# Optimization experiments

Measured on AMD Instinct MI355X. Metric: run time of the kernel, lower is better.

The kernel has to match this reference:

```python
import jax, jax.numpy as jnp
import numpy as np

N = 50000
E = 800000
F_IN = 256
HID = 96
N_CLS = 32
NEG_SLOPE = 0.2


def setup_inputs() -> dict:
    key = jax.random.key(0)
    ks = jax.random.split(key, 10)
    x = jax.random.normal(ks[0], (N, F_IN), dtype=jnp.float32)
    edge_index = jax.random.randint(ks[1], (2, E), 0, N, dtype=jnp.int64)
    s1 = 1.0 / np.sqrt(F_IN)
    s2 = 1.0 / np.sqrt(HID)
    return {
        "x": x,
        "edge_index": edge_index,
        "W1": jax.random.normal(ks[2], (F_IN, HID), dtype=jnp.float32) * s1,
        "a1_src": jax.random.normal(ks[3], (HID,), dtype=jnp.float32) * s2,
        "a1_dst": jax.random.normal(ks[4], (HID,), dtype=jnp.float32) * s2,
        "b1": jnp.zeros((HID,), dtype=jnp.float32),
        "W2": jax.random.normal(ks[5], (HID, N_CLS), dtype=jnp.float32) * s2,
        "a2_src": jax.random.normal(ks[6], (N_CLS,), dtype=jnp.float32) * (1.0 / np.sqrt(N_CLS)),
        "a2_dst": jax.random.normal(ks[7], (N_CLS,), dtype=jnp.float32) * (1.0 / np.sqrt(N_CLS)),
        "b2": jnp.zeros((N_CLS,), dtype=jnp.float32),
    }


def _gat_conv(x, src, dst, W, a_src, a_dst, b, n_nodes):
    # single-head GATConv (PyG defaults), self-loops already in src/dst
    h = x @ W                                  # [N, out]
    alpha_src = h @ a_src                      # [N]
    alpha_dst = h @ a_dst                      # [N]
    e = alpha_src[src] + alpha_dst[dst]        # [E'] edge logits (msg j->i: dst groups)
    e = jnp.where(e > 0, e, NEG_SLOPE * e)     # leaky_relu
    # segment softmax over edges grouped by destination node
    m = jax.ops.segment_max(e, dst, num_segments=n_nodes)
    ex = jnp.exp(e - m[dst])
    denom = jax.ops.segment_sum(ex, dst, num_segments=n_nodes)
    alpha = ex / denom[dst]                    # [E']
    out = jax.ops.segment_sum(alpha[:, None] * h[src], dst, num_segments=n_nodes)
    return out + b


def reference(x, edge_index, W1, a1_src, a1_dst, b1, W2, a2_src, a2_dst, b2):
    loops = jnp.arange(N, dtype=edge_index.dtype)
    src = jnp.concatenate([edge_index[0], loops])
    dst = jnp.concatenate([edge_index[1], loops])
    h = _gat_conv(x, src, dst, W1, a1_src, a1_dst, b1, N)
    h = jax.nn.elu(h)
    # dropout omitted (eval mode, training=False)
    out = _gat_conv(h, src, dst, W2, a2_src, a2_dst, b2, N)
    return jax.nn.log_softmax(out, axis=1)
```

## Files before the change

### kernel.cpp

```cpp
#include <hip/hip_runtime.h>
#include <cstdint>
#include <cstddef>

#define NNODES 50000
#define NEDGES 800000
#define MEDGES (NEDGES + NNODES)
#define FIN    256
#define HID    96
#define NCLS   32
#define NEG_SLOPE 0.2f

#define NBUCK  391
#define BCAP   3072

typedef unsigned int uint32;
typedef __attribute__((ext_vector_type(8))) short short8;
typedef __attribute__((ext_vector_type(4))) float f32x4;

__device__ __forceinline__ ushort bf_round(float f) {
    uint32 u = __float_as_uint(f);
    u += 0x7FFFu + ((u >> 16) & 1u);
    return (ushort)(u >> 16);
}
__device__ __forceinline__ uint32 pack_bf16x2(float a, float b) {
    return (uint32)bf_round(a) | ((uint32)bf_round(b) << 16);
}
__device__ __forceinline__ float bf_lo(uint32 u) { return __uint_as_float(u << 16); }
__device__ __forceinline__ float bf_hi(uint32 u) { return __uint_as_float(u & 0xFFFF0000u); }
__device__ __forceinline__ float lrelu(float t) { return (t > 0.f) ? t : NEG_SLOPE * t; }
__device__ __forceinline__ float af(int i) { return __int_as_float(i); }


__global__ __launch_bounds__(256) void bucket1_kernel(const int* __restrict__ ei,
                                                      int* __restrict__ gcount,
                                                      int2* __restrict__ staging) {
    __shared__ int hist[NBUCK];
    __shared__ int base_sh[NBUCK];
    for (int i = threadIdx.x; i < NBUCK; i += 256) hist[i] = 0;
    __syncthreads();

    int s[8], d[8], rk[8], bk[8];
    int e0 = blockIdx.x * 2048;
#pragma unroll
    for (int i = 0; i < 8; ++i) {
        int e = e0 + i * 256 + threadIdx.x;
        if (e < MEDGES) {
            if (e < NEDGES) { s[i] = ei[e]; d[i] = ei[NEDGES + e]; }
            else            { s[i] = e - NEDGES; d[i] = s[i]; }
            bk[i] = d[i] >> 7;
            rk[i] = atomicAdd(&hist[bk[i]], 1);
        } else bk[i] = -1;
    }
    __syncthreads();
    for (int i = threadIdx.x; i < NBUCK; i += 256) {
        int c = hist[i];
        base_sh[i] = c ? atomicAdd(&gcount[i], c) : 0;
    }
    __syncthreads();
#pragma unroll
    for (int i = 0; i < 8; ++i) {
        if (bk[i] >= 0) {
            int pos = base_sh[bk[i]] + rk[i];
            if (pos < BCAP)
                staging[(size_t)bk[i] * BCAP + pos] = make_int2(s[i], d[i]);
        }
    }
}

__global__ __launch_bounds__(512) void bscan_kernel(const int* __restrict__ gcount,
                                                    int* __restrict__ bbase) {
    __shared__ int sd[512];
    int t = threadIdx.x;
    int v = (t < NBUCK) ? gcount[t] : 0;
    sd[t] = v;
    __syncthreads();
    for (int off = 1; off < 512; off <<= 1) {
        int val = (t >= off) ? sd[t - off] : 0;
        __syncthreads();
        sd[t] += val;
        __syncthreads();
    }
    if (t < NBUCK) bbase[t] = sd[t] - v;
}

__global__ __launch_bounds__(256) void bucket2_kernel(const int2* __restrict__ staging,
                                                      const int* __restrict__ gcount,
                                                      const int* __restrict__ bbase,
                                                      int* __restrict__ rowptr,
                                                      int* __restrict__ esrc) {
    __shared__ int dcount[128];
    __shared__ int dincl[128];
    __shared__ int dexcl[128];
    __shared__ int fillc[128];

    const int b     = blockIdx.x;
    const int t     = threadIdx.x;
    const int cnt   = gcount[b];
    const int ebase = bbase[b];
    const int node0 = b << 7;
    const int2* st  = staging + (size_t)b * BCAP;

    for (int i = t; i < 128; i += 256) { dcount[i] = 0; fillc[i] = 0; }
    __syncthreads();

    for (int i = t; i < cnt; i += 256)
        atomicAdd(&dcount[st[i].y - node0], 1);
    __syncthreads();

    if (t < 128) dincl[t] = dcount[t];
    __syncthreads();
    for (int off = 1; off < 128; off <<= 1) {
        int val = (t >= off && t < 128) ? dincl[t - off] : 0;
        __syncthreads();
        if (t < 128) dincl[t] += val;
        __syncthreads();
    }
    if (t < 128) {
        int excl = dincl[t] - dcount[t];
        dexcl[t] = excl;
        int node = node0 + t;
        if (node < NNODES) rowptr[node] = ebase + excl;
    }
    if (b == NBUCK - 1 && t == 0) rowptr[NNODES] = MEDGES;
    __syncthreads();

    for (int i = t; i < cnt; i += 256) {
        int2 sd2 = st[i];
        int dd = sd2.y - node0;
        int r = atomicAdd(&fillc[dd], 1);
        esrc[ebase + dexcl[dd] + r] = sd2.x;
    }
}


__global__ __launch_bounds__(256) void packw_kernel(const float* __restrict__ W1,
                                                    const float* __restrict__ W2,
                                                    ushort* __restrict__ W1p,
                                                    ushort* __restrict__ W2p) {
    for (int idx = threadIdx.x; idx < 6 * 8 * 64 * 8; idx += 256) {
        int j     = idx & 7;
        int lane  = (idx >> 3) & 63;
        int kstep = (idx >> 9) & 7;
        int ntile = idx >> 12;
        int k = kstep * 32 + ((lane >> 4) << 3) + j;
        int n = ntile * 16 + (lane & 15);
        W1p[idx] = bf_round(W1[(size_t)k * 96 + n]);
    }
    for (int idx = threadIdx.x; idx < 2 * 3 * 64 * 8; idx += 256) {
        int j     = idx & 7;
        int lane  = (idx >> 3) & 63;
        int kstep = (idx >> 9) % 3;
        int ntile = (idx >> 9) / 3;
        int k = kstep * 32 + ((lane >> 4) << 3) + j;
        int n = ntile * 16 + (lane & 15);
        W2p[idx] = bf_round(W2[(size_t)k * 32 + n]);
    }
}


__global__ __launch_bounds__(256) void gemm1_kernel(const float* __restrict__ x,
                                                    const ushort* __restrict__ W1p,
                                                    const float* __restrict__ a_src,
                                                    const float* __restrict__ a_dst,
                                                    ushort* __restrict__ h1,
                                                    float* __restrict__ as1,
                                                    float* __restrict__ ad1) {
    const int tid  = threadIdx.x;
    const int lane = tid & 63;
    const int wv   = tid >> 6;
    const int m    = lane & 15;
    const int quad = lane >> 4;
    const int node0 = blockIdx.x * 64;

    int arow = node0 + wv * 16 + m;
    if (arow >= NNODES) arow = NNODES - 1;
    const float* xr = x + (size_t)arow * FIN + quad * 8;

    const short8* Wp = (const short8*)W1p;

    f32x4 acc[6];
#pragma unroll
    for (int t = 0; t < 6; ++t) acc[t] = (f32x4){0.f, 0.f, 0.f, 0.f};

#pragma unroll
    for (int ks = 0; ks < 8; ++ks) {
        float4 v0 = *(const float4*)(xr + ks * 32);
        float4 v1 = *(const float4*)(xr + ks * 32 + 4);
        short8 a;
        a[0] = (short)bf_round(v0.x); a[1] = (short)bf_round(v0.y);
        a[2] = (short)bf_round(v0.z); a[3] = (short)bf_round(v0.w);
        a[4] = (short)bf_round(v1.x); a[5] = (short)bf_round(v1.y);
        a[6] = (short)bf_round(v1.z); a[7] = (short)bf_round(v1.w);
#pragma unroll
        for (int t = 0; t < 6; ++t) {
            short8 b = Wp[(t * 8 + ks) * 64 + lane];
            acc[t] = __builtin_amdgcn_mfma_f32_16x16x32_bf16(a, b, acc[t], 0, 0, 0);
        }
    }

    float as_reg[6], ad_reg[6];
#pragma unroll
    for (int t = 0; t < 6; ++t) {
        as_reg[t] = a_src[t * 16 + m];
        ad_reg[t] = a_dst[t * 16 + m];
    }

#pragma unroll
    for (int r = 0; r < 4; ++r) {
        int node = node0 + wv * 16 + quad * 4 + r;
        float ps = 0.f, pd = 0.f;
#pragma unroll
        for (int t = 0; t < 6; ++t) {
            ps += acc[t][r] * as_reg[t];
            pd += acc[t][r] * ad_reg[t];
        }
#pragma unroll
        for (int off = 1; off < 16; off <<= 1) {
            ps += __shfl_xor(ps, off);
            pd += __shfl_xor(pd, off);
        }
        if (node < NNODES) {
            ushort* hp = h1 + (size_t)node * 96 + m;
#pragma unroll
            for (int t = 0; t < 6; ++t) hp[t * 16] = bf_round(acc[t][r]);
            if (m == 0) { as1[node] = ps; ad1[node] = pd; }
        }
    }
}


__global__ __launch_bounds__(256) void gemm2_kernel(const uint32* __restrict__ y48,
                                                    const ushort* __restrict__ W2p,
                                                    const float* __restrict__ a_src,
                                                    const float* __restrict__ a_dst,
                                                    float* __restrict__ h2,
                                                    float* __restrict__ as2,
                                                    float* __restrict__ ad2) {
    const int tid  = threadIdx.x;
    const int lane = tid & 63;
    const int wv   = tid >> 6;
    const int m    = lane & 15;
    const int quad = lane >> 4;
    const int node0 = blockIdx.x * 64;

    int arow = node0 + wv * 16 + m;
    if (arow >= NNODES) arow = NNODES - 1;
    const short8* Ar = (const short8*)(y48 + (size_t)arow * 48);
    const short8* Wp = (const short8*)W2p;

    f32x4 acc[2];
    acc[0] = (f32x4){0.f, 0.f, 0.f, 0.f};
    acc[1] = (f32x4){0.f, 0.f, 0.f, 0.f};

#pragma unroll
    for (int ks = 0; ks < 3; ++ks) {
        short8 a = Ar[ks * 4 + quad];
#pragma unroll
        for (int t = 0; t < 2; ++t) {
            short8 b = Wp[(t * 3 + ks) * 64 + lane];
            acc[t] = __builtin_amdgcn_mfma_f32_16x16x32_bf16(a, b, acc[t], 0, 0, 0);
        }
    }

    float as_reg[2], ad_reg[2];
#pragma unroll
    for (int t = 0; t < 2; ++t) {
        as_reg[t] = a_src[t * 16 + m];
        ad_reg[t] = a_dst[t * 16 + m];
    }

#pragma unroll
    for (int r = 0; r < 4; ++r) {
        int node = node0 + wv * 16 + quad * 4 + r;
        float ps = 0.f, pd = 0.f;
#pragma unroll
        for (int t = 0; t < 2; ++t) {
            ps += acc[t][r] * as_reg[t];
            pd += acc[t][r] * ad_reg[t];
        }
#pragma unroll
        for (int off = 1; off < 16; off <<= 1) {
            ps += __shfl_xor(ps, off);
            pd += __shfl_xor(pd, off);
        }
        if (node < NNODES) {
            float* hp = h2 + (size_t)node * 32 + m;
            hp[0]  = acc[0][r];
            hp[16] = acc[1][r];
            if (m == 0) { as2[node] = ps; ad2[node] = pd; }
        }
    }
}


__global__ __launch_bounds__(256) void agg96_kernel(const ushort* __restrict__ h,
                                                    const float* __restrict__ asrc,
                                                    const float* __restrict__ adst,
                                                    const float* __restrict__ bias,
                                                    const int* __restrict__ rowptr,
                                                    const int* __restrict__ esrc,
                                                    uint32* __restrict__ out1b) {
    __shared__ int2 sa[4][64];
    int wave = threadIdx.x >> 6;
    int lane = threadIdx.x & 63;
    int i = blockIdx.x * 4 + wave;
    if (i >= NNODES) return;

    int start = rowptr[i], end = rowptr[i + 1];
    int deg = end - start;
    float ad = adst[i];
    int fl = (lane < 48) ? lane : 47;

    float acc0 = 0.f, acc1 = 0.f;

    if (deg <= 64) {
        int p = start + lane;
        bool valid = p < end;
        int s_reg = valid ? esrc[p] : 0;
        float e = -1e30f;
        if (valid) e = lrelu(asrc[s_reg] + ad);
        float mx = e;
#pragma unroll
        for (int off = 32; off; off >>= 1) mx = fmaxf(mx, __shfl_xor(mx, off));
        float ex = valid ? __expf(e - mx) : 0.f;
        float sum = ex;
#pragma unroll
        for (int off = 32; off; off >>= 1) sum += __shfl_xor(sum, off);
        float a_reg = ex / sum;

        sa[wave][lane] = make_int2(s_reg, __float_as_int(a_reg));
        const int4* sap = (const int4*)&sa[wave][0];

        int eb = 0;
        for (; eb + 8 <= deg; eb += 8) {
            int4 q0 = sap[(eb >> 1) + 0];
            int4 q1 = sap[(eb >> 1) + 1];
            int4 q2 = sap[(eb >> 1) + 2];
            int4 q3 = sap[(eb >> 1) + 3];
            uint32 u0 = ((const uint32*)(h + (size_t)q0.x * 96))[fl];
            uint32 u1 = ((const uint32*)(h + (size_t)q0.z * 96))[fl];
            uint32 u2 = ((const uint32*)(h + (size_t)q1.x * 96))[fl];
            uint32 u3 = ((const uint32*)(h + (size_t)q1.z * 96))[fl];
            uint32 u4 = ((const uint32*)(h + (size_t)q2.x * 96))[fl];
            uint32 u5 = ((const uint32*)(h + (size_t)q2.z * 96))[fl];
            uint32 u6 = ((const uint32*)(h + (size_t)q3.x * 96))[fl];
            uint32 u7 = ((const uint32*)(h + (size_t)q3.z * 96))[fl];
            acc0 += af(q0.y) * bf_lo(u0) + af(q0.w) * bf_lo(u1)
                  + af(q1.y) * bf_lo(u2) + af(q1.w) * bf_lo(u3)
                  + af(q2.y) * bf_lo(u4) + af(q2.w) * bf_lo(u5)
                  + af(q3.y) * bf_lo(u6) + af(q3.w) * bf_lo(u7);
            acc1 += af(q0.y) * bf_hi(u0) + af(q0.w) * bf_hi(u1)
                  + af(q1.y) * bf_hi(u2) + af(q1.w) * bf_hi(u3)
                  + af(q2.y) * bf_hi(u4) + af(q2.w) * bf_hi(u5)
                  + af(q3.y) * bf_hi(u6) + af(q3.w) * bf_hi(u7);
        }
        for (; eb + 2 <= deg; eb += 2) {
            int4 q = sap[eb >> 1];
            uint32 u0 = ((const uint32*)(h + (size_t)q.x * 96))[fl];
            uint32 u1 = ((const uint32*)(h + (size_t)q.z * 96))[fl];
            acc0 += af(q.y) * bf_lo(u0) + af(q.w) * bf_lo(u1);
            acc1 += af(q.y) * bf_hi(u0) + af(q.w) * bf_hi(u1);
        }
        if (eb < deg) {
            int2 q = sa[wave][eb];
            uint32 u = ((const uint32*)(h + (size_t)q.x * 96))[fl];
            acc0 += af(q.y) * bf_lo(u);
            acc1 += af(q.y) * bf_hi(u);
        }
    } else {
        float mx = -1e30f;
        for (int p = start + lane; p < end; p += 64)
            mx = fmaxf(mx, lrelu(asrc[esrc[p]] + ad));
#pragma unroll
        for (int off = 32; off; off >>= 1) mx = fmaxf(mx, __shfl_xor(mx, off));
        float sum = 0.f;
        for (int p = start + lane; p < end; p += 64)
            sum += __expf(lrelu(asrc[esrc[p]] + ad) - mx);
#pragma unroll
        for (int off = 32; off; off >>= 1) sum += __shfl_xor(sum, off);
        float inv = 1.f / sum;
        for (int p = start; p < end; ++p) {
            int s = esrc[p];
            float a = __expf(lrelu(asrc[s] + ad) - mx) * inv;
            uint32 u = ((const uint32*)(h + (size_t)s * 96))[fl];
            acc0 += a * bf_lo(u);
            acc1 += a * bf_hi(u);
        }
    }

    if (lane < 48) {
        float v0 = acc0 + bias[2 * lane];
        v0 = (v0 > 0.f) ? v0 : expm1f(v0);
        float v1 = acc1 + bias[2 * lane + 1];
        v1 = (v1 > 0.f) ? v1 : expm1f(v1);
        out1b[(size_t)i * 48 + lane] = pack_bf16x2(v0, v1);
    }
}


__global__ __launch_bounds__(256) void agg32_kernel(const float* __restrict__ h,
                                                    const float* __restrict__ asrc,
                                                    const float* __restrict__ adst,
                                                    const float* __restrict__ bias,
                                                    const int* __restrict__ rowptr,
                                                    const int* __restrict__ esrc,
                                                    float* __restrict__ out) {
    __shared__ int2 sa[4][64];
    int wave = threadIdx.x >> 6;
    int lane = threadIdx.x & 63;
    int i = blockIdx.x * 4 + wave;
    if (i >= NNODES) return;

    int e2 = lane >> 5;
    int f  = lane & 31;

    int start = rowptr[i], end = rowptr[i + 1];
    int deg = end - start;
    float ad = adst[i];

    float acc = 0.f;

    if (deg <= 64) {
        int p = start + lane;
        bool valid = p < end;
        int s_reg = valid ? esrc[p] : 0;
        float e = -1e30f;
        if (valid) e = lrelu(asrc[s_reg] + ad);
        float mx = e;
#pragma unroll
        for (int off = 32; off; off >>= 1) mx = fmaxf(mx, __shfl_xor(mx, off));
        float ex = valid ? __expf(e - mx) : 0.f;
        float sum = ex;
#pragma unroll
        for (int off = 32; off; off >>= 1) sum += __shfl_xor(sum, off);
        float a_reg = ex / sum;

        sa[wave][lane] = make_int2(s_reg, __float_as_int(a_reg));
        const int4* sap = (const int4*)&sa[wave][0];

        int eb = 0;
        for (; eb + 8 <= deg; eb += 8) {
            int4 q0 = sap[(eb >> 1) + 0];
            int4 q1 = sap[(eb >> 1) + 1];
            int4 q2 = sap[(eb >> 1) + 2];
            int4 q3 = sap[(eb >> 1) + 3];
            int   s0 = e2 ? q0.z : q0.x;  float a0 = af(e2 ? q0.w : q0.y);
            int   s1 = e2 ? q1.z : q1.x;  float a1 = af(e2 ? q1.w : q1.y);
            int   s2 = e2 ? q2.z : q2.x;  float a2 = af(e2 ? q2.w : q2.y);
            int   s3 = e2 ? q3.z : q3.x;  float a3 = af(e2 ? q3.w : q3.y);
            float v0 = h[(size_t)s0 * 32 + f];
            float v1 = h[(size_t)s1 * 32 + f];
            float v2 = h[(size_t)s2 * 32 + f];
            float v3 = h[(size_t)s3 * 32 + f];
            acc += a0 * v0 + a1 * v1 + a2 * v2 + a3 * v3;
        }
        for (; eb + 2 <= deg; eb += 2) {
            int4 q = sap[eb >> 1];
            int   s = e2 ? q.z : q.x;
            float a = af(e2 ? q.w : q.y);
            acc += a * h[(size_t)s * 32 + f];
        }
        if (eb < deg) {
            int2 q = sa[wave][eb];
            float a = (e2 == 0) ? af(q.y) : 0.f;
            acc += a * h[(size_t)q.x * 32 + f];
        }
        acc += __shfl_xor(acc, 32);
    } else {
        float mx = -1e30f;
        for (int p = start + lane; p < end; p += 64)
            mx = fmaxf(mx, lrelu(asrc[esrc[p]] + ad));
#pragma unroll
        for (int off = 32; off; off >>= 1) mx = fmaxf(mx, __shfl_xor(mx, off));
        float sum = 0.f;
        for (int p = start + lane; p < end; p += 64)
            sum += __expf(lrelu(asrc[esrc[p]] + ad) - mx);
#pragma unroll
        for (int off = 32; off; off >>= 1) sum += __shfl_xor(sum, off);
        float inv = 1.f / sum;
        for (int p = start + e2; p < end; p += 2) {
            int s = esrc[p];
            float a = __expf(lrelu(asrc[s] + ad) - mx) * inv;
            acc += a * h[(size_t)s * 32 + f];
        }
        acc += __shfl_xor(acc, 32);
    }

    float z = acc + bias[f];
    float m2 = z;
#pragma unroll
    for (int off = 16; off; off >>= 1) m2 = fmaxf(m2, __shfl_xor(m2, off));
    float ex = __expf(z - m2);
    float s2 = ex;
#pragma unroll
    for (int off = 16; off; off >>= 1) s2 += __shfl_xor(s2, off);
    if (lane < 32) out[(size_t)i * 32 + f] = z - m2 - logf(s2);
}


extern "C" void kernel_launch(void* const* d_in, const int* in_sizes, int n_in,
                              void* d_out, int out_size, void* d_ws, size_t ws_size,
                              hipStream_t stream) {
    const float* x   = (const float*)d_in[0];
    const int*   ei  = (const int*)d_in[1];
    const float* W1  = (const float*)d_in[2];
    const float* a1s = (const float*)d_in[3];
    const float* a1d = (const float*)d_in[4];
    const float* b1  = (const float*)d_in[5];
    const float* W2  = (const float*)d_in[6];
    const float* a2s = (const float*)d_in[7];
    const float* a2d = (const float*)d_in[8];
    const float* b2  = (const float*)d_in[9];
    float* out = (float*)d_out;

    size_t off = 0;
    auto alloc = [&](size_t bytes) {
        void* p = (char*)d_ws + off;
        off += (bytes + 255) & ~(size_t)255;
        return p;
    };
    ushort* h1    = (ushort*)alloc((size_t)NNODES * HID * 2);
    uint32* out1b = (uint32*)alloc((size_t)NNODES * 48 * 4);
    int2* staging = (int2*)alloc((size_t)NBUCK * BCAP * 8);
    float* as1    = (float*)alloc((size_t)NNODES * 4);
    float* ad1    = (float*)alloc((size_t)NNODES * 4);
    float* as2    = (float*)alloc((size_t)NNODES * 4);
    float* ad2    = (float*)alloc((size_t)NNODES * 4);
    int*   rowptr = (int*)alloc((size_t)(NNODES + 1) * 4);
    int*   esrc   = (int*)alloc((size_t)MEDGES * 4);
    ushort* W1p   = (ushort*)alloc((size_t)6 * 8 * 64 * 8 * 2);
    ushort* W2p   = (ushort*)alloc((size_t)2 * 3 * 64 * 8 * 2);
    int*   gcount = (int*)alloc((size_t)NBUCK * 4);
    int*   bbase  = (int*)alloc((size_t)NBUCK * 4);
    float* h2     = (float*)h1;

    hipMemsetAsync(gcount, 0, (size_t)NBUCK * 4, stream);

    const int nbB1   = (MEDGES + 2047) / 2048;
    const int nbGemm = (NNODES + 63) / 64;
    const int nbAgg  = (NNODES + 3) / 4;

    packw_kernel<<<1, 256, 0, stream>>>(W1, W2, W1p, W2p);
    bucket1_kernel<<<nbB1, 256, 0, stream>>>(ei, gcount, staging);
    bscan_kernel<<<1, 512, 0, stream>>>(gcount, bbase);
    bucket2_kernel<<<NBUCK, 256, 0, stream>>>(staging, gcount, bbase, rowptr, esrc);

    gemm1_kernel<<<nbGemm, 256, 0, stream>>>(x, W1p, a1s, a1d, h1, as1, ad1);
    agg96_kernel<<<nbAgg, 256, 0, stream>>>(h1, as1, ad1, b1, rowptr, esrc, out1b);

    gemm2_kernel<<<nbGemm, 256, 0, stream>>>(out1b, W2p, a2s, a2d, h2, as2, ad2);
    agg32_kernel<<<nbAgg, 256, 0, stream>>>(h2, as2, ad2, b2, rowptr, esrc, out);
}
```

Measured before the change: 234.8 us.

## Pack staging edges, store layer-2 features as bf16, vectorize aggregation gathers

Result: no change. 237.5 us (+1.1%).

```diff
diff --git a/kernel.cpp b/kernel.cpp
--- a/kernel.cpp
+++ b/kernel.cpp
@@ -33,21 +33,23 @@
 
 __global__ __launch_bounds__(256) void bucket1_kernel(const int* __restrict__ ei,
                                                       int* __restrict__ gcount,
-                                                      int2* __restrict__ staging) {
+                                                      int* __restrict__ staging) {
     __shared__ int hist[NBUCK];
     __shared__ int base_sh[NBUCK];
     for (int i = threadIdx.x; i < NBUCK; i += 256) hist[i] = 0;
     __syncthreads();
 
-    int s[8], d[8], rk[8], bk[8];
+    int v[8], rk[8], bk[8];
     int e0 = blockIdx.x * 2048;
 #pragma unroll
     for (int i = 0; i < 8; ++i) {
         int e = e0 + i * 256 + threadIdx.x;
         if (e < MEDGES) {
-            if (e < NEDGES) { s[i] = ei[e]; d[i] = ei[NEDGES + e]; }
-            else            { s[i] = e - NEDGES; d[i] = s[i]; }
-            bk[i] = d[i] >> 7;
+            int s, d;
+            if (e < NEDGES) { s = ei[e]; d = ei[NEDGES + e]; }
+            else            { s = e - NEDGES; d = s; }
+            bk[i] = d >> 7;
+            v[i]  = s | ((d & 127) << 16);
             rk[i] = atomicAdd(&hist[bk[i]], 1);
         } else bk[i] = -1;
     }
@@ -62,7 +64,7 @@
         if (bk[i] >= 0) {
             int pos = base_sh[bk[i]] + rk[i];
             if (pos < BCAP)
-                staging[(size_t)bk[i] * BCAP + pos] = make_int2(s[i], d[i]);
+                staging[(size_t)bk[i] * BCAP + pos] = v[i];
         }
     }
 }
@@ -83,7 +85,7 @@
     if (t < NBUCK) bbase[t] = sd[t] - v;
 }
 
-__global__ __launch_bounds__(256) void bucket2_kernel(const int2* __restrict__ staging,
+__global__ __launch_bounds__(256) void bucket2_kernel(const int* __restrict__ staging,
                                                       const int* __restrict__ gcount,
                                                       const int* __restrict__ bbase,
                                                       int* __restrict__ rowptr,
@@ -98,13 +100,13 @@
     const int cnt   = gcount[b];
     const int ebase = bbase[b];
     const int node0 = b << 7;
-    const int2* st  = staging + (size_t)b * BCAP;
+    const int* st   = staging + (size_t)b * BCAP;
 
     for (int i = t; i < 128; i += 256) { dcount[i] = 0; fillc[i] = 0; }
     __syncthreads();
 
     for (int i = t; i < cnt; i += 256)
-        atomicAdd(&dcount[st[i].y - node0], 1);
+        atomicAdd(&dcount[st[i] >> 16], 1);
     __syncthreads();
 
     if (t < 128) dincl[t] = dcount[t];
@@ -125,10 +127,10 @@
     __syncthreads();
 
     for (int i = t; i < cnt; i += 256) {
-        int2 sd2 = st[i];
-        int dd = sd2.y - node0;
+        int v = st[i];
+        int dd = v >> 16;
         int r = atomicAdd(&fillc[dd], 1);
-        esrc[ebase + dexcl[dd] + r] = sd2.x;
+        esrc[ebase + dexcl[dd] + r] = v & 0xFFFF;
     }
 }
 
@@ -233,7 +235,7 @@
                                                     const ushort* __restrict__ W2p,
                                                     const float* __restrict__ a_src,
                                                     const float* __restrict__ a_dst,
-                                                    float* __restrict__ h2,
+                                                    uint32* __restrict__ h2b,
                                                     float* __restrict__ as2,
                                                     float* __restrict__ ad2) {
     const int tid  = threadIdx.x;
@@ -284,9 +286,7 @@
             pd += __shfl_xor(pd, off);
         }
         if (node < NNODES) {
-            float* hp = h2 + (size_t)node * 32 + m;
-            hp[0]  = acc[0][r];
-            hp[16] = acc[1][r];
+            h2b[(size_t)node * 16 + m] = pack_bf16x2(acc[0][r], acc[1][r]);
             if (m == 0) { as2[node] = ps; ad2[node] = pd; }
         }
     }
@@ -309,16 +309,12 @@
     int start = rowptr[i], end = rowptr[i + 1];
     int deg = end - start;
     float ad = adst[i];
-    int fl = (lane < 48) ? lane : 47;
-
-    float acc0 = 0.f, acc1 = 0.f;
 
     if (deg <= 64) {
         int p = start + lane;
         bool valid = p < end;
         int s_reg = valid ? esrc[p] : 0;
-        float e = -1e30f;
-        if (valid) e = lrelu(asrc[s_reg] + ad);
+        float e = valid ? lrelu(asrc[s_reg] + ad) : -1e30f;
         float mx = e;
 #pragma unroll
         for (int off = 32; off; off >>= 1) mx = fmaxf(mx, __shfl_xor(mx, off));
@@ -326,48 +322,52 @@
         float sum = ex;
 #pragma unroll
         for (int off = 32; off; off >>= 1) sum += __shfl_xor(sum, off);
-        float a_reg = ex / sum;
-
-        sa[wave][lane] = make_int2(s_reg, __float_as_int(a_reg));
-        const int4* sap = (const int4*)&sa[wave][0];
-
-        int eb = 0;
-        for (; eb + 8 <= deg; eb += 8) {
-            int4 q0 = sap[(eb >> 1) + 0];
-            int4 q1 = sap[(eb >> 1) + 1];
-            int4 q2 = sap[(eb >> 1) + 2];
-            int4 q3 = sap[(eb >> 1) + 3];
-            uint32 u0 = ((const uint32*)(h + (size_t)q0.x * 96))[fl];
-            uint32 u1 = ((const uint32*)(h + (size_t)q0.z * 96))[fl];
-            uint32 u2 = ((const uint32*)(h + (size_t)q1.x * 96))[fl];
-            uint32 u3 = ((const uint32*)(h + (size_t)q1.z * 96))[fl];
-            uint32 u4 = ((const uint32*)(h + (size_t)q2.x * 96))[fl];
-            uint32 u5 = ((const uint32*)(h + (size_t)q2.z * 96))[fl];
-            uint32 u6 = ((const uint32*)(h + (size_t)q3.x * 96))[fl];
-            uint32 u7 = ((const uint32*)(h + (size_t)q3.z * 96))[fl];
-            acc0 += af(q0.y) * bf_lo(u0) + af(q0.w) * bf_lo(u1)
-                  + af(q1.y) * bf_lo(u2) + af(q1.w) * bf_lo(u3)
-                  + af(q2.y) * bf_lo(u4) + af(q2.w) * bf_lo(u5)
-                  + af(q3.y) * bf_lo(u6) + af(q3.w) * bf_lo(u7);
-            acc1 += af(q0.y) * bf_hi(u0) + af(q0.w) * bf_hi(u1)
-                  + af(q1.y) * bf_hi(u2) + af(q1.w) * bf_hi(u3)
-                  + af(q2.y) * bf_hi(u4) + af(q2.w) * bf_hi(u5)
-                  + af(q3.y) * bf_hi(u6) + af(q3.w) * bf_hi(u7);
-        }
-        for (; eb + 2 <= deg; eb += 2) {
-            int4 q = sap[eb >> 1];
-            uint32 u0 = ((const uint32*)(h + (size_t)q.x * 96))[fl];
-            uint32 u1 = ((const uint32*)(h + (size_t)q.z * 96))[fl];
-            acc0 += af(q.y) * bf_lo(u0) + af(q.w) * bf_lo(u1);
-            acc1 += af(q.y) * bf_hi(u0) + af(q.w) * bf_hi(u1);
-        }
-        if (eb < deg) {
-            int2 q = sa[wave][eb];
-            uint32 u = ((const uint32*)(h + (size_t)q.x * 96))[fl];
-            acc0 += af(q.y) * bf_lo(u);
-            acc1 += af(q.y) * bf_hi(u);
+        sa[wave][lane] = make_int2(s_reg, __float_as_int(ex / sum));
+
+        const int q   = lane >> 4;
+        const int fl  = lane & 15;
+        const int flc = (fl < 12) ? fl : 11;
+        float acc[8];
+#pragma unroll
+        for (int j = 0; j < 8; ++j) acc[j] = 0.f;
+
+#pragma unroll 2
+        for (int eb = 0; eb < deg; eb += 4) {
+            int e0 = eb + q;
+            int2 qq = sa[wave][(e0 < 64) ? e0 : 63];
+            float a = (fl < 12 && e0 < deg) ? af(qq.y) : 0.f;
+            const uint4* hr = (const uint4*)(h + (size_t)qq.x * 96);
+            uint4 u = hr[flc];
+            acc[0] = fmaf(a, bf_lo(u.x), acc[0]);
+            acc[1] = fmaf(a, bf_hi(u.x), acc[1]);
+            acc[2] = fmaf(a, bf_lo(u.y), acc[2]);
+            acc[3] = fmaf(a, bf_hi(u.y), acc[3]);
+            acc[4] = fmaf(a, bf_lo(u.z), acc[4]);
+            acc[5] = fmaf(a, bf_hi(u.z), acc[5]);
+            acc[6] = fmaf(a, bf_lo(u.w), acc[6]);
+            acc[7] = fmaf(a, bf_hi(u.w), acc[7]);
+        }
+#pragma unroll
+        for (int j = 0; j < 8; ++j) {
+            acc[j] += __shfl_xor(acc[j], 16);
+            acc[j] += __shfl_xor(acc[j], 32);
+        }
+        if (lane < 12) {
+            float v[8];
+#pragma unroll
+            for (int j = 0; j < 8; ++j) {
+                float t = acc[j] + bias[8 * lane + j];
+                v[j] = (t > 0.f) ? t : expm1f(t);
+            }
+            uint4 o;
+            o.x = pack_bf16x2(v[0], v[1]);
+            o.y = pack_bf16x2(v[2], v[3]);
+            o.z = pack_bf16x2(v[4], v[5]);
+            o.w = pack_bf16x2(v[6], v[7]);
+            *(uint4*)(out1b + (size_t)i * 48 + 4 * lane) = o;
         }
     } else {
+        int fl47 = (lane < 48) ? lane : 47;
         float mx = -1e30f;
         for (int p = start + lane; p < end; p += 64)
             mx = fmaxf(mx, lrelu(asrc[esrc[p]] + ad));
@@ -379,26 +379,26 @@
 #pragma unroll
         for (int off = 32; off; off >>= 1) sum += __shfl_xor(sum, off);
         float inv = 1.f / sum;
+        float acc0 = 0.f, acc1 = 0.f;
         for (int p = start; p < end; ++p) {
             int s = esrc[p];
             float a = __expf(lrelu(asrc[s] + ad) - mx) * inv;
-            uint32 u = ((const uint32*)(h + (size_t)s * 96))[fl];
+            uint32 u = ((const uint32*)(h + (size_t)s * 96))[fl47];
             acc0 += a * bf_lo(u);
             acc1 += a * bf_hi(u);
         }
-    }
-
-    if (lane < 48) {
-        float v0 = acc0 + bias[2 * lane];
-        v0 = (v0 > 0.f) ? v0 : expm1f(v0);
-        float v1 = acc1 + bias[2 * lane + 1];
-        v1 = (v1 > 0.f) ? v1 : expm1f(v1);
-        out1b[(size_t)i * 48 + lane] = pack_bf16x2(v0, v1);
-    }
-}
-
-
-__global__ __launch_bounds__(256) void agg32_kernel(const float* __restrict__ h,
+        if (lane < 48) {
+            float v0 = acc0 + bias[2 * lane];
+            v0 = (v0 > 0.f) ? v0 : expm1f(v0);
+            float v1 = acc1 + bias[2 * lane + 1];
+            v1 = (v1 > 0.f) ? v1 : expm1f(v1);
+            out1b[(size_t)i * 48 + lane] = pack_bf16x2(v0, v1);
+        }
+    }
+}
+
+
+__global__ __launch_bounds__(256) void agg32_kernel(const uint32* __restrict__ h2b,
                                                     const float* __restrict__ asrc,
                                                     const float* __restrict__ adst,
                                                     const float* __restrict__ bias,
@@ -411,21 +411,15 @@
     int i = blockIdx.x * 4 + wave;
     if (i >= NNODES) return;
 
-    int e2 = lane >> 5;
-    int f  = lane & 31;
-
     int start = rowptr[i], end = rowptr[i + 1];
     int deg = end - start;
     float ad = adst[i];
-
-    float acc = 0.f;
 
     if (deg <= 64) {
         int p = start + lane;
         bool valid = p < end;
         int s_reg = valid ? esrc[p] : 0;
-        float e = -1e30f;
-        if (valid) e = lrelu(asrc[s_reg] + ad);
+        float e = valid ? lrelu(asrc[s_reg] + ad) : -1e30f;
         float mx = e;
 #pragma unroll
         for (int off = 32; off; off >>= 1) mx = fmaxf(mx, __shfl_xor(mx, off));
@@ -433,40 +427,54 @@
         float sum = ex;
 #pragma unroll
         for (int off = 32; off; off >>= 1) sum += __shfl_xor(sum, off);
-        float a_reg = ex / sum;
-
-        sa[wave][lane] = make_int2(s_reg, __float_as_int(a_reg));
-        const int4* sap = (const int4*)&sa[wave][0];
-
-        int eb = 0;
-        for (; eb + 8 <= deg; eb += 8) {
-            int4 q0 = sap[(eb >> 1) + 0];
-            int4 q1 = sap[(eb >> 1) + 1];
-            int4 q2 = sap[(eb >> 1) + 2];
-            int4 q3 = sap[(eb >> 1) + 3];
-            int   s0 = e2 ? q0.z : q0.x;  float a0 = af(e2 ? q0.w : q0.y);
-            int   s1 = e2 ? q1.z : q1.x;  float a1 = af(e2 ? q1.w : q1.y);
-            int   s2 = e2 ? q2.z : q2.x;  float a2 = af(e2 ? q2.w : q2.y);
-            int   s3 = e2 ? q3.z : q3.x;  float a3 = af(e2 ? q3.w : q3.y);
-            float v0 = h[(size_t)s0 * 32 + f];
-            float v1 = h[(size_t)s1 * 32 + f];
-            float v2 = h[(size_t)s2 * 32 + f];
-            float v3 = h[(size_t)s3 * 32 + f];
-            acc += a0 * v0 + a1 * v1 + a2 * v2 + a3 * v3;
-        }
-        for (; eb + 2 <= deg; eb += 2) {
-            int4 q = sap[eb >> 1];
-            int   s = e2 ? q.z : q.x;
-            float a = af(e2 ? q.w : q.y);
-            acc += a * h[(size_t)s * 32 + f];
-        }
-        if (eb < deg) {
-            int2 q = sa[wave][eb];
-            float a = (e2 == 0) ? af(q.y) : 0.f;
-            acc += a * h[(size_t)q.x * 32 + f];
-        }
-        acc += __shfl_xor(acc, 32);
+        sa[wave][lane] = make_int2(s_reg, __float_as_int(ex / sum));
+
+        const int g  = lane >> 3;
+        const int fl = lane & 7;
+        float acc[4];
+#pragma unroll
+        for (int j = 0; j < 4; ++j) acc[j] = 0.f;
+
+#pragma unroll 2
+        for (int eb = 0; eb < deg; eb += 8) {
+            int e0 = eb + g;
+            int2 qq = sa[wave][(e0 < 64) ? e0 : 63];
+            float a = (e0 < deg) ? af(qq.y) : 0.f;
+            const uint2* hr = (const uint2*)(h2b + (size_t)qq.x * 16);
+            uint2 u = hr[fl];
+            acc[0] = fmaf(a, bf_lo(u.x), acc[0]);
+            acc[1] = fmaf(a, bf_hi(u.x), acc[1]);
+            acc[2] = fmaf(a, bf_lo(u.y), acc[2]);
+            acc[3] = fmaf(a, bf_hi(u.y), acc[3]);
+        }
+#pragma unroll
+        for (int j = 0; j < 4; ++j) {
+            acc[j] += __shfl_xor(acc[j], 8);
+            acc[j] += __shfl_xor(acc[j], 16);
+            acc[j] += __shfl_xor(acc[j], 32);
+        }
+
+        float z0 = acc[0] + bias[2 * fl];
+        float z1 = acc[1] + bias[2 * fl + 16];
+        float z2 = acc[2] + bias[2 * fl + 1];
+        float z3 = acc[3] + bias[2 * fl + 17];
+        float m2 = fmaxf(fmaxf(z0, z1), fmaxf(z2, z3));
+#pragma unroll
+        for (int off = 4; off; off >>= 1) m2 = fmaxf(m2, __shfl_xor(m2, off));
+        float s2 = __expf(z0 - m2) + __expf(z1 - m2) + __expf(z2 - m2) + __expf(z3 - m2);
+#pragma unroll
+        for (int off = 4; off; off >>= 1) s2 += __shfl_xor(s2, off);
+        float ls = m2 + logf(s2);
+        if (lane < 8) {
+            float* op = out + (size_t)i * 32;
+            op[2 * fl]      = z0 - ls;
+            op[2 * fl + 16] = z1 - ls;
+            op[2 * fl + 1]  = z2 - ls;
+            op[2 * fl + 17] = z3 - ls;
+        }
     } else {
+        int e2 = lane >> 5;
+        int f  = lane & 31;
         float mx = -1e30f;
         for (int p = start + lane; p < end; p += 64)
             mx = fmaxf(mx, lrelu(asrc[esrc[p]] + ad));
@@ -478,23 +486,25 @@
 #pragma unroll
         for (int off = 32; off; off >>= 1) sum += __shfl_xor(sum, off);
         float inv = 1.f / sum;
+        float acc = 0.f;
         for (int p = start + e2; p < end; p += 2) {
             int s = esrc[p];
             float a = __expf(lrelu(asrc[s] + ad) - mx) * inv;
-            acc += a * h[(size_t)s * 32 + f];
+            uint32 u = h2b[(size_t)s * 16 + (f & 15)];
+            acc += a * ((f < 16) ? bf_lo(u) : bf_hi(u));
         }
         acc += __shfl_xor(acc, 32);
-    }
-
-    float z = acc + bias[f];
-    float m2 = z;
-#pragma unroll
-    for (int off = 16; off; off >>= 1) m2 = fmaxf(m2, __shfl_xor(m2, off));
-    float ex = __expf(z - m2);
-    float s2 = ex;
-#pragma unroll
-    for (int off = 16; off; off >>= 1) s2 += __shfl_xor(s2, off);
-    if (lane < 32) out[(size_t)i * 32 + f] = z - m2 - logf(s2);
+
+        float z = acc + bias[f];
+        float m2 = z;
+#pragma unroll
+        for (int off = 16; off; off >>= 1) m2 = fmaxf(m2, __shfl_xor(m2, off));
+        float ex2 = __expf(z - m2);
+        float s2 = ex2;
+#pragma unroll
+        for (int off = 16; off; off >>= 1) s2 += __shfl_xor(s2, off);
+        if (lane < 32) out[(size_t)i * 32 + f] = z - m2 - logf(s2);
+    }
 }
 
 
@@ -521,7 +531,7 @@
     };
     ushort* h1    = (ushort*)alloc((size_t)NNODES * HID * 2);
     uint32* out1b = (uint32*)alloc((size_t)NNODES * 48 * 4);
-    int2* staging = (int2*)alloc((size_t)NBUCK * BCAP * 8);
+    int*  staging = (int*)alloc((size_t)NBUCK * BCAP * 4);
     float* as1    = (float*)alloc((size_t)NNODES * 4);
     float* ad1    = (float*)alloc((size_t)NNODES * 4);
     float* as2    = (float*)alloc((size_t)NNODES * 4);
@@ -532,7 +542,7 @@
     ushort* W2p   = (ushort*)alloc((size_t)2 * 3 * 64 * 8 * 2);
     int*   gcount = (int*)alloc((size_t)NBUCK * 4);
     int*   bbase  = (int*)alloc((size_t)NBUCK * 4);
-    float* h2     = (float*)h1;
+    uint32* h2b   = (uint32*)h1;
 
     hipMemsetAsync(gcount, 0, (size_t)NBUCK * 4, stream);
 
@@ -548,6 +558,6 @@
     gemm1_kernel<<<nbGemm, 256, 0, stream>>>(x, W1p, a1s, a1d, h1, as1, ad1);
     agg96_kernel<<<nbAgg, 256, 0, stream>>>(h1, as1, ad1, b1, rowptr, esrc, out1b);
 
-    gemm2_kernel<<<nbGemm, 256, 0, stream>>>(out1b, W2p, a2s, a2d, h2, as2, ad2);
-    agg32_kernel<<<nbAgg, 256, 0, stream>>>(h2, as2, ad2, b2, rowptr, esrc, out);
-}
+    gemm2_kernel<<<nbGemm, 256, 0, stream>>>(out1b, W2p, a2s, a2d, h2b, as2, ad2);
+    agg32_kernel<<<nbAgg, 256, 0, stream>>>(h2b, as2, ad2, b2, rowptr, esrc, out);
+}
```
